# Kernel tuning notes

Measured on AMD Instinct MI355X. Metric: run time of the kernel, lower is better.

Reference implementation:

```python
import jax, jax.numpy as jnp
import numpy as np

DIM = 1024
HEADS = 16
HD = DIM // HEADS  # 64
EPS = 1.1920928955078125e-07  # torch.finfo(float32).eps, RMSNorm default


def setup_inputs() -> dict:
    key = jax.random.key(0)
    ks = jax.random.split(key, 8)
    s = 0.02
    return {
        "x": jax.random.normal(ks[0], (2, 2048, DIM), jnp.float32),
        "pe": jax.random.normal(ks[1], (1, 1, 2048, HD // 2, 2, 2), jnp.float32),
        "qkv_w": jax.random.normal(ks[2], (3 * DIM, DIM), jnp.float32) * s,
        "qkv_b": jax.random.normal(ks[3], (3 * DIM,), jnp.float32) * s,
        "q_norm_w": jnp.ones((HD,), jnp.float32),
        "k_norm_w": jnp.ones((HD,), jnp.float32),
        "proj_w": jax.random.normal(ks[4], (DIM, DIM), jnp.float32) * s,
        "proj_b": jax.random.normal(ks[5], (DIM,), jnp.float32) * s,
    }


def _rms_norm(t, w):
    var = jnp.mean(jnp.square(t), axis=-1, keepdims=True)
    return t * jax.lax.rsqrt(var + EPS) * w


def _apply_rope(t, pe):
    # t: [B,H,L,D]; pe: [1,1,L,D/2,2,2]
    B, H, L, D = t.shape
    tp = t.reshape(B, H, L, D // 2, 1, 2)
    out = pe[..., 0] * tp[..., 0] + pe[..., 1] * tp[..., 1]  # [B,H,L,D/2,2]
    return out.reshape(B, H, L, D)


def reference(x, pe, qkv_w, qkv_b, q_norm_w, k_norm_w, proj_w, proj_b):
    B, L, _ = x.shape
    qkv = x @ qkv_w.T + qkv_b  # [B,L,3*DIM]
    qkv = qkv.reshape(B, L, 3, HEADS, HD).transpose(2, 0, 3, 1, 4)  # [3,B,H,L,D]
    q, k, v = qkv[0], qkv[1], qkv[2]
    q = _rms_norm(q, q_norm_w)
    k = _rms_norm(k, k_norm_w)
    q = _apply_rope(q, pe)
    k = _apply_rope(k, pe)
    scale = 1.0 / np.sqrt(HD).astype(np.float32)
    scores = jnp.einsum("bhqd,bhkd->bhqk", q, k) * scale  # [B,H,L,L]
    attn = jax.nn.softmax(scores, axis=-1)
    o = jnp.einsum("bhqk,bhkd->bhqd", attn, v)  # [B,H,L,D]
    o = o.transpose(0, 2, 1, 3).reshape(B, L, DIM)  # B L (H D)
    return o @ proj_w.T + proj_b
```

## Files before the change

### kernel.cpp

```cpp
#include <hip/hip_runtime.h>
#include <hip/hip_bf16.h>

#define DIM   1024
#define HEADS 16
#define HD    64
#define BB    2
#define LL    2048
#define MTOT  (BB*LL)
#define EPSV  1.1920928955078125e-07f

typedef __attribute__((ext_vector_type(8))) short bf16x8;
typedef __attribute__((ext_vector_type(4))) float f32x4;
typedef unsigned short ushort_t;

__device__ __forceinline__ float bf2f(ushort_t u) {
    unsigned int x = ((unsigned int)u) << 16;
    return __builtin_bit_cast(float, x);
}
__device__ __forceinline__ ushort_t f2bf(float f) {
    unsigned int x = __builtin_bit_cast(unsigned int, f);
    unsigned int r = (x + 0x7FFFu + ((x >> 16) & 1u)) >> 16;
    return (ushort_t)r;
}

__global__ __launch_bounds__(256) void f32_to_bf16_k(const float* __restrict__ in,
                                                     ushort_t* __restrict__ out, int n) {
    int i = (blockIdx.x * 256 + threadIdx.x) * 4;
    if (i < n) {
        float4 v = *(const float4*)(in + i);
        ushort4 o;
        o.x = f2bf(v.x); o.y = f2bf(v.y); o.z = f2bf(v.z); o.w = f2bf(v.w);
        *(ushort4*)(out + i) = o;
    }
}

__global__ __launch_bounds__(512, 2) void gemm256(const ushort_t* __restrict__ A,
                                                  const ushort_t* __restrict__ Bt,
                                                  const float* __restrict__ bias,
                                                  ushort_t* __restrict__ C,
                                                  int M, int N, int K) {
    __shared__ __attribute__((aligned(16))) ushort_t Asm[2][256 * 64];
    __shared__ __attribute__((aligned(16))) ushort_t Bsm[2][256 * 64];
    const int tid = threadIdx.x;
    const int lane = tid & 63, wid = tid >> 6;
    const int wm = wid >> 1, wn = wid & 1;
    const int r = lane & 15, g = lane >> 4;

    const int mtiles = M >> 8;
    const int cpx = gridDim.x >> 3;
    const int bid = blockIdx.x;
    const int swz = (bid & 7) * cpx + (bid >> 3);
    const int mt = swz % mtiles, nt = swz / mtiles;
    const int m0 = mt * 256, n0 = nt * 256;

    int srow[2], sgx[2];
#pragma unroll
    for (int q = 0; q < 2; ++q) {
        int c = q * 512 + tid;
        srow[q] = c >> 3;
        sgx[q] = ((c & 7) ^ (srow[q] & 7)) * 8;
    }
    const ushort_t* pa[2][2];
    const ushort_t* pb[2][2];
#pragma unroll
    for (int q = 0; q < 2; ++q)
#pragma unroll
        for (int h = 0; h < 2; ++h) {
            pa[q][h] = A + (size_t)(m0 + h * 128 + srow[q]) * K + sgx[q];
            pb[q][h] = Bt + (size_t)(n0 + h * 128 + srow[q]) * K + sgx[q];
        }

    f32x4 acc[4][8] = {};

    auto stage = [&](int kt, int slot) {
        const int kc = kt * 64;
#pragma unroll
        for (int h = 0; h < 2; ++h)
#pragma unroll
            for (int q = 0; q < 2; ++q) {
                __builtin_amdgcn_global_load_lds(
                    (const __attribute__((address_space(1))) void*)(pa[q][h] + kc),
                    (__attribute__((address_space(3))) void*)(&Asm[slot][0] + h * 8192 + (q * 512 + wid * 64) * 8),
                    16, 0, 0);
                __builtin_amdgcn_global_load_lds(
                    (const __attribute__((address_space(1))) void*)(pb[q][h] + kc),
                    (__attribute__((address_space(3))) void*)(&Bsm[slot][0] + h * 8192 + (q * 512 + wid * 64) * 8),
                    16, 0, 0);
            }
    };

    stage(0, 0);
    asm volatile("s_waitcnt vmcnt(0)" ::: "memory");
    __builtin_amdgcn_s_barrier();
    asm volatile("" ::: "memory");

    const int nkt = K >> 6;
    for (int kt = 0; kt < nkt; ++kt) {
        const int slot = kt & 1;
        if (kt + 1 < nkt) stage(kt + 1, slot ^ 1);
        const ushort_t* As = &Asm[slot][0];
        const ushort_t* Bs = &Bsm[slot][0];
#pragma unroll
        for (int ks = 0; ks < 2; ++ks) {
            bf16x8 af[4], bf[8];
#pragma unroll
            for (int mi = 0; mi < 4; ++mi) {
                int row = wm * 64 + mi * 16 + r;
                af[mi] = *(const bf16x8*)(As + row * 64 + (((ks * 4 + g) * 8) ^ ((row & 7) * 8)));
            }
#pragma unroll
            for (int ni = 0; ni < 8; ++ni) {
                int row = wn * 128 + ni * 16 + r;
                bf[ni] = *(const bf16x8*)(Bs + row * 64 + (((ks * 4 + g) * 8) ^ ((row & 7) * 8)));
            }
            __builtin_amdgcn_s_setprio(1);
#pragma unroll
            for (int mi = 0; mi < 4; ++mi)
#pragma unroll
                for (int ni = 0; ni < 8; ++ni)
                    acc[mi][ni] = __builtin_amdgcn_mfma_f32_16x16x32_bf16(af[mi], bf[ni], acc[mi][ni], 0, 0, 0);
            __builtin_amdgcn_s_setprio(0);
        }
        asm volatile("s_waitcnt vmcnt(0)" ::: "memory");
        __builtin_amdgcn_s_barrier();
        asm volatile("" ::: "memory");
    }

#pragma unroll
    for (int ni = 0; ni < 8; ++ni) {
        int col = n0 + wn * 128 + ni * 16 + r;
        float bv = bias[col];
#pragma unroll
        for (int mi = 0; mi < 4; ++mi)
#pragma unroll
            for (int reg = 0; reg < 4; ++reg) {
                int row = m0 + wm * 64 + mi * 16 + g * 4 + reg;
                C[(size_t)row * N + col] = f2bf(acc[mi][ni][reg] + bv);
            }
    }
}

template <int OUT_BF16>
__global__ __launch_bounds__(256) void gemm_bt(const ushort_t* __restrict__ A,
                                               const ushort_t* __restrict__ Bt,
                                               const float* __restrict__ bias,
                                               void* __restrict__ Cout,
                                               int M, int N, int K) {
    __shared__ __attribute__((aligned(16))) ushort_t Asm[128 * 32];
    __shared__ __attribute__((aligned(16))) ushort_t Bsm[128 * 32];
    int tid = threadIdx.x;
    int lane = tid & 63, wid = tid >> 6;
    int wm = wid >> 1, wn = wid & 1;
    int r = lane & 15, g = lane >> 4;
    int m0 = blockIdx.y * 128, n0 = blockIdx.x * 128;

    f32x4 acc[4][4] = {};

    int niter = K >> 5;
    for (int kk = 0; kk < niter; ++kk) {
        int k0 = kk << 5;
        __syncthreads();
#pragma unroll
        for (int p = 0; p < 2; ++p) {
            int off = (p * 256 + tid) * 8;
            int row = off >> 5, col = off & 31;
            int ldsoff = (p * 256 + wid * 64) * 8;
            __builtin_amdgcn_global_load_lds(
                (const __attribute__((address_space(1))) void*)(A + (size_t)(m0 + row) * K + k0 + col),
                (__attribute__((address_space(3))) void*)(Asm + ldsoff), 16, 0, 0);
            __builtin_amdgcn_global_load_lds(
                (const __attribute__((address_space(1))) void*)(Bt + (size_t)(n0 + row) * K + k0 + col),
                (__attribute__((address_space(3))) void*)(Bsm + ldsoff), 16, 0, 0);
        }
        __syncthreads();
        bf16x8 af[4], bfr[4];
#pragma unroll
        for (int mi = 0; mi < 4; mi++)
            af[mi] = *(const bf16x8*)(Asm + (wm * 64 + mi * 16 + r) * 32 + g * 8);
#pragma unroll
        for (int ni = 0; ni < 4; ni++)
            bfr[ni] = *(const bf16x8*)(Bsm + (wn * 64 + ni * 16 + r) * 32 + g * 8);
#pragma unroll
        for (int mi = 0; mi < 4; mi++)
#pragma unroll
            for (int ni = 0; ni < 4; ni++)
                acc[mi][ni] = __builtin_amdgcn_mfma_f32_16x16x32_bf16(af[mi], bfr[ni], acc[mi][ni], 0, 0, 0);
    }
#pragma unroll
    for (int mi = 0; mi < 4; mi++)
#pragma unroll
        for (int ni = 0; ni < 4; ni++) {
            int col = n0 + wn * 64 + ni * 16 + r;
            float bv = bias[col];
#pragma unroll
            for (int reg = 0; reg < 4; reg++) {
                int row = m0 + wm * 64 + mi * 16 + g * 4 + reg;
                float v = acc[mi][ni][reg] + bv;
                if (OUT_BF16)
                    ((ushort_t*)Cout)[(size_t)row * N + col] = f2bf(v);
                else
                    ((float*)Cout)[(size_t)row * N + col] = v;
            }
        }
}

__global__ __launch_bounds__(256) void norm_rope_k(const ushort_t* __restrict__ qkv,
                                                   const float* __restrict__ pe,
                                                   const float* __restrict__ qnw,
                                                   const float* __restrict__ knw,
                                                   ushort_t* __restrict__ qh,
                                                   ushort_t* __restrict__ kh,
                                                   ushort_t* __restrict__ vT) {
    __shared__ ushort_t T[64][68];
    const int tid = threadIdx.x;
    const int lane = tid & 63, w = tid >> 6;
    const int rg = lane >> 4;
    const int d4 = (lane & 15) * 4;
    const int l0 = blockIdx.x * 64;
    const int t  = blockIdx.y;
    const int bh = blockIdx.z;
    const int b = bh >> 4, h = bh & 15;

    if (t == 2) {
#pragma unroll
        for (int i = 0; i < 4; ++i) {
            int ll = w * 16 + rg + 4 * i;
            int m = b * 2048 + l0 + ll;
            ushort4 v = *(const ushort4*)(qkv + (size_t)m * 3072 + 2048 + h * 64 + d4);
            *(ushort4*)(&T[ll][d4]) = v;
        }
        __syncthreads();
        const int d = tid >> 2, lq = (tid & 3) * 16;
        ushort_t* dst = vT + ((size_t)(bh * 64 + d)) * 2048 + l0 + lq;
#pragma unroll
        for (int c = 0; c < 4; ++c) {
            ushort4 o;
            o.x = T[lq + c * 4 + 0][d];
            o.y = T[lq + c * 4 + 1][d];
            o.z = T[lq + c * 4 + 2][d];
            o.w = T[lq + c * 4 + 3][d];
            *(ushort4*)(dst + c * 4) = o;
        }
        return;
    }

    const float* nwp = (t == 0) ? qnw : knw;
    const float4 nwv = *(const float4*)(nwp + d4);
    ushort_t* dst = (t == 0) ? qh : kh;
    const float qscale = (t == 0) ? 0.125f : 1.0f;
#pragma unroll
    for (int i = 0; i < 4; ++i) {
        int ll = w * 16 + rg + 4 * i;
        int l = l0 + ll;
        int m = b * 2048 + l;
        ushort4 vv = *(const ushort4*)(qkv + (size_t)m * 3072 + t * 1024 + h * 64 + d4);
        float v0 = bf2f(vv.x), v1 = bf2f(vv.y), v2 = bf2f(vv.z), v3 = bf2f(vv.w);
        float ss = v0 * v0 + v1 * v1 + v2 * v2 + v3 * v3;
        ss += __shfl_xor(ss, 1, 64);
        ss += __shfl_xor(ss, 2, 64);
        ss += __shfl_xor(ss, 4, 64);
        ss += __shfl_xor(ss, 8, 64);
        float rms = rsqrtf(ss * (1.0f / 64.0f) + EPSV);
        v0 *= rms * nwv.x; v1 *= rms * nwv.y; v2 *= rms * nwv.z; v3 *= rms * nwv.w;
        float4 p0 = *(const float4*)(pe + (size_t)l * 128 + 2 * d4);
        float4 p1 = *(const float4*)(pe + (size_t)l * 128 + 2 * d4 + 4);
        float o0 = (p0.x * v0 + p0.y * v1) * qscale;
        float o1 = (p0.z * v0 + p0.w * v1) * qscale;
        float o2 = (p1.x * v2 + p1.y * v3) * qscale;
        float o3 = (p1.z * v2 + p1.w * v3) * qscale;
        ushort4 o;
        o.x = f2bf(o0); o.y = f2bf(o1); o.z = f2bf(o2); o.w = f2bf(o3);
        *(ushort4*)(dst + ((size_t)bh * 2048 + l) * 64 + d4) = o;
    }
}

__global__ __launch_bounds__(256, 2) void attn_k(const ushort_t* __restrict__ qh,
                                                 const ushort_t* __restrict__ kh,
                                                 const ushort_t* __restrict__ vT,
                                                 ushort_t* __restrict__ ob) {
    __shared__ __attribute__((aligned(16))) ushort_t Ksm[2][64 * 64];
    __shared__ __attribute__((aligned(16))) ushort_t Vsm[2][64 * 64];
    __shared__ __attribute__((aligned(16))) ushort_t Plds[4][2][16 * 64];

    const int tid = threadIdx.x;
    const int lane = tid & 63, wid = tid >> 6;
    const int r = lane & 15, g = lane >> 4;
    const int qt = blockIdx.x, bh = blockIdx.y;
    const int q0 = qt * 128 + wid * 32;
    const ushort_t* Q  = qh + (size_t)bh * LL * 64;
    const ushort_t* Kb = kh + (size_t)bh * LL * 64;
    const ushort_t* Vt = vT + (size_t)bh * 64 * LL;

    int row_[2], ccx_[2];
#pragma unroll
    for (int q = 0; q < 2; ++q) {
        int c = q * 256 + tid;
        row_[q] = c >> 3;
        ccx_[q] = (c & 7) ^ (row_[q] & 7);
    }
    const int swz = (r & 7) * 8;

    bf16x8 qf[2][2];
#pragma unroll
    for (int mf = 0; mf < 2; ++mf)
#pragma unroll
        for (int hf = 0; hf < 2; ++hf)
            qf[mf][hf] = *(const bf16x8*)(Q + (size_t)(q0 + mf * 16 + r) * 64 + hf * 32 + g * 8);

    f32x4 acc[2][4] = {};
    float mrow[2] = {-1e30f, -1e30f};
    float srow[2] = {0.f, 0.f};
    const f32x4 zero = {};

#pragma unroll
    for (int q = 0; q < 2; ++q) {
        __builtin_amdgcn_global_load_lds(
            (const __attribute__((address_space(1))) void*)(Kb + (size_t)row_[q] * 64 + ccx_[q] * 8),
            (__attribute__((address_space(3))) void*)(&Ksm[0][0] + (q * 256 + wid * 64) * 8), 16, 0, 0);
        __builtin_amdgcn_global_load_lds(
            (const __attribute__((address_space(1))) void*)(Vt + (size_t)row_[q] * 2048 + ccx_[q] * 8),
            (__attribute__((address_space(3))) void*)(&Vsm[0][0] + (q * 256 + wid * 64) * 8), 16, 0, 0);
    }
    __syncthreads();

    int buf = 0;
    for (int it = 0; it < 32; ++it) {
        if (it < 31) {
            int kvn = (it + 1) * 64;
#pragma unroll
            for (int q = 0; q < 2; ++q) {
                __builtin_amdgcn_global_load_lds(
                    (const __attribute__((address_space(1))) void*)(Kb + (size_t)(kvn + row_[q]) * 64 + ccx_[q] * 8),
                    (__attribute__((address_space(3))) void*)(&Ksm[buf ^ 1][0] + (q * 256 + wid * 64) * 8), 16, 0, 0);
                __builtin_amdgcn_global_load_lds(
                    (const __attribute__((address_space(1))) void*)(Vt + (size_t)row_[q] * 2048 + kvn + ccx_[q] * 8),
                    (__attribute__((address_space(3))) void*)(&Vsm[buf ^ 1][0] + (q * 256 + wid * 64) * 8), 16, 0, 0);
            }
        }
        const ushort_t* Kl = &Ksm[buf][0];
        const ushort_t* Vl = &Vsm[buf][0];

        bf16x8 kf[4][2];
#pragma unroll
        for (int kt = 0; kt < 4; ++kt)
#pragma unroll
            for (int hf = 0; hf < 2; ++hf)
                kf[kt][hf] = *(const bf16x8*)(Kl + (kt * 16 + r) * 64 + (((hf * 4 + g) * 8) ^ swz));

        f32x4 s[2][4];
        __builtin_amdgcn_s_setprio(1);
#pragma unroll
        for (int mf = 0; mf < 2; ++mf)
#pragma unroll
            for (int kt = 0; kt < 4; ++kt) {
                f32x4 t0 = __builtin_amdgcn_mfma_f32_16x16x32_bf16(kf[kt][0], qf[mf][0], zero, 0, 0, 0);
                s[mf][kt] = __builtin_amdgcn_mfma_f32_16x16x32_bf16(kf[kt][1], qf[mf][1], t0, 0, 0, 0);
            }
        __builtin_amdgcn_s_setprio(0);

#pragma unroll
        for (int mf = 0; mf < 2; ++mf) {
            float pm = -1e30f;
#pragma unroll
            for (int kt = 0; kt < 4; ++kt)
#pragma unroll
                for (int reg = 0; reg < 4; ++reg) pm = fmaxf(pm, s[mf][kt][reg]);
            pm = fmaxf(pm, __shfl_xor(pm, 16, 64));
            pm = fmaxf(pm, __shfl_xor(pm, 32, 64));
            bool skip = (__all(pm <= mrow[mf] + 8.0f) != 0);
            float mn, al;
            if (skip) {
                mn = mrow[mf];
            } else {
                mn = fmaxf(mrow[mf], pm);
                al = __expf(mrow[mf] - mn);
                mrow[mf] = mn;
            }
            float rs = 0.f;
#pragma unroll
            for (int kt = 0; kt < 4; ++kt)
#pragma unroll
                for (int reg = 0; reg < 4; ++reg) {
                    float p = __expf(s[mf][kt][reg] - mn);
                    s[mf][kt][reg] = p;
                    rs += p;
                }
            rs += __shfl_xor(rs, 16, 64);
            rs += __shfl_xor(rs, 32, 64);
            if (skip) {
                srow[mf] += rs;
            } else {
                srow[mf] = srow[mf] * al + rs;
                float ab[4];
#pragma unroll
                for (int reg = 0; reg < 4; ++reg) ab[reg] = __shfl(al, g * 4 + reg, 16);
#pragma unroll
                for (int dt = 0; dt < 4; ++dt)
#pragma unroll
                    for (int reg = 0; reg < 4; ++reg) acc[mf][dt][reg] *= ab[reg];
            }
#pragma unroll
            for (int kt = 0; kt < 4; ++kt) {
                ushort4 pw;
                pw.x = f2bf(s[mf][kt][0]); pw.y = f2bf(s[mf][kt][1]);
                pw.z = f2bf(s[mf][kt][2]); pw.w = f2bf(s[mf][kt][3]);
                *(ushort4*)(&Plds[wid][mf][0] + r * 64 + (((2 * kt + (g >> 1)) * 8) ^ swz) + (g & 1) * 4) = pw;
            }
        }
        asm volatile("s_waitcnt lgkmcnt(0)" ::: "memory");
        __builtin_amdgcn_sched_barrier(0);

        bf16x8 pa[2][2];
#pragma unroll
        for (int mf = 0; mf < 2; ++mf)
#pragma unroll
            for (int hf = 0; hf < 2; ++hf)
                pa[mf][hf] = *(const bf16x8*)(&Plds[wid][mf][0] + r * 64 + (((hf * 4 + g) * 8) ^ swz));

        __builtin_amdgcn_s_setprio(1);
#pragma unroll
        for (int dt = 0; dt < 4; ++dt)
#pragma unroll
            for (int hv = 0; hv < 2; ++hv) {
                bf16x8 vf = *(const bf16x8*)(Vl + (dt * 16 + r) * 64 + (((hv * 4 + g) * 8) ^ swz));
#pragma unroll
                for (int mf = 0; mf < 2; ++mf)
                    acc[mf][dt] = __builtin_amdgcn_mfma_f32_16x16x32_bf16(pa[mf][hv], vf, acc[mf][dt], 0, 0, 0);
            }
        __builtin_amdgcn_s_setprio(0);

        __syncthreads();
        buf ^= 1;
    }

    int b = bh >> 4, h = bh & 15;
#pragma unroll
    for (int mf = 0; mf < 2; ++mf) {
        float sinv = 1.0f / srow[mf];
        float sb[4];
#pragma unroll
        for (int reg = 0; reg < 4; ++reg) sb[reg] = __shfl(sinv, g * 4 + reg, 16);
#pragma unroll
        for (int dt = 0; dt < 4; ++dt)
#pragma unroll
            for (int reg = 0; reg < 4; ++reg) {
                int l = q0 + mf * 16 + g * 4 + reg;
                ob[((size_t)(b * 2048 + l)) * 1024 + h * 64 + dt * 16 + r] =
                    f2bf(acc[mf][dt][reg] * sb[reg]);
            }
    }
}

extern "C" void kernel_launch(void* const* d_in, const int* in_sizes, int n_in,
                              void* d_out, int out_size, void* d_ws, size_t ws_size,
                              hipStream_t stream) {
    const float* x      = (const float*)d_in[0];
    const float* pe     = (const float*)d_in[1];
    const float* qkv_w  = (const float*)d_in[2];
    const float* qkv_b  = (const float*)d_in[3];
    const float* qnw    = (const float*)d_in[4];
    const float* knw    = (const float*)d_in[5];
    const float* proj_w = (const float*)d_in[6];
    const float* proj_b = (const float*)d_in[7];
    float* out = (float*)d_out;

    char* ws = (char*)d_ws;
    ushort_t* xb    = (ushort_t*)(ws);
    ushort_t* wqkv  = (ushort_t*)(ws + 8388608);
    ushort_t* wproj = (ushort_t*)(ws + 8388608 + 6291456);
    ushort_t* qkvb  = (ushort_t*)(ws + 16777216);
    ushort_t* qhp   = (ushort_t*)(ws + 16777216 + 25165824);
    ushort_t* khp   = (ushort_t*)(ws + 16777216 + 25165824 + 8388608);
    ushort_t* vtp   = (ushort_t*)(ws + 16777216 + 25165824 + 2 * 8388608);
    ushort_t* obp   = qkvb;

    f32_to_bf16_k<<<MTOT * DIM / 1024, 256, 0, stream>>>(x, xb, MTOT * DIM);
    f32_to_bf16_k<<<3 * DIM * DIM / 1024, 256, 0, stream>>>(qkv_w, wqkv, 3 * DIM * DIM);
    f32_to_bf16_k<<<DIM * DIM / 1024, 256, 0, stream>>>(proj_w, wproj, DIM * DIM);

    gemm256<<<(MTOT / 256) * (3 * DIM / 256), 512, 0, stream>>>(xb, wqkv, qkv_b, qkvb,
                                                                MTOT, 3 * DIM, DIM);
    norm_rope_k<<<dim3(32, 3, 32), 256, 0, stream>>>(qkvb, pe, qnw, knw, qhp, khp, vtp);
    attn_k<<<dim3(16, 32), 256, 0, stream>>>(qhp, khp, vtp, obp);
    gemm_bt<0><<<dim3(DIM / 128, MTOT / 128), 256, 0, stream>>>(obp, wproj, proj_b, out,
                                                                MTOT, DIM, DIM);
}
```

Measured before the change: 234.6 us.

## Retile QKV and projection GEMMs, merge conversions, pack bf16 converts in attention

The three fp32-to-bf16 conversion launches become one kernel. The 256x256 QKV GEMM is replaced by a 128x128 double-buffered tile kernel, giving 768 blocks instead of 192 for better CU coverage. The projection GEMM gains a 128x64 tile with a 64-wide K step, swizzled LDS and double buffering, producing 512 blocks. The attention kernel now packs P to bf16 with v_cvt_pk_bf16_f32. In exchange, smaller tiles lower per-block arithmetic intensity and raise global/LDS traffic per FLOP.

Result: faster. 217.6 us (-7.2%).

```diff
diff --git a/kernel.cpp b/kernel.cpp
--- a/kernel.cpp
+++ b/kernel.cpp
@@ -22,71 +22,71 @@
     unsigned int r = (x + 0x7FFFu + ((x >> 16) & 1u)) >> 16;
     return (ushort_t)r;
 }
-
-__global__ __launch_bounds__(256) void f32_to_bf16_k(const float* __restrict__ in,
-                                                     ushort_t* __restrict__ out, int n) {
+__device__ __forceinline__ unsigned int cvt_pk_bf16(float lo, float hi) {
+    unsigned int r;
+    asm("v_cvt_pk_bf16_f32 %0, %1, %2" : "=v"(r) : "v"(lo), "v"(hi));
+    return r;
+}
+
+__global__ __launch_bounds__(256) void cvt_all_k(const float* __restrict__ a, int na,
+                                                 const float* __restrict__ b, int nb,
+                                                 const float* __restrict__ c,
+                                                 ushort_t* __restrict__ oa,
+                                                 ushort_t* __restrict__ ob,
+                                                 ushort_t* __restrict__ oc) {
     int i = (blockIdx.x * 256 + threadIdx.x) * 4;
-    if (i < n) {
-        float4 v = *(const float4*)(in + i);
-        ushort4 o;
-        o.x = f2bf(v.x); o.y = f2bf(v.y); o.z = f2bf(v.z); o.w = f2bf(v.w);
-        *(ushort4*)(out + i) = o;
-    }
-}
-
-__global__ __launch_bounds__(512, 2) void gemm256(const ushort_t* __restrict__ A,
+    const float* src;
+    ushort_t* dst;
+    int off;
+    if (i < na)            { src = a; dst = oa; off = i; }
+    else if (i < na + nb)  { src = b; dst = ob; off = i - na; }
+    else                   { src = c; dst = oc; off = i - na - nb; }
+    float4 v = *(const float4*)(src + off);
+    ushort4 o;
+    o.x = f2bf(v.x); o.y = f2bf(v.y); o.z = f2bf(v.z); o.w = f2bf(v.w);
+    *(ushort4*)(dst + off) = o;
+}
+
+__global__ __launch_bounds__(256, 2) void gemm128(const ushort_t* __restrict__ A,
                                                   const ushort_t* __restrict__ Bt,
                                                   const float* __restrict__ bias,
                                                   ushort_t* __restrict__ C,
                                                   int M, int N, int K) {
-    __shared__ __attribute__((aligned(16))) ushort_t Asm[2][256 * 64];
-    __shared__ __attribute__((aligned(16))) ushort_t Bsm[2][256 * 64];
+    __shared__ __attribute__((aligned(16))) ushort_t Asm[2][128 * 64];
+    __shared__ __attribute__((aligned(16))) ushort_t Bsm[2][128 * 64];
     const int tid = threadIdx.x;
     const int lane = tid & 63, wid = tid >> 6;
     const int wm = wid >> 1, wn = wid & 1;
     const int r = lane & 15, g = lane >> 4;
-
-    const int mtiles = M >> 8;
-    const int cpx = gridDim.x >> 3;
-    const int bid = blockIdx.x;
-    const int swz = (bid & 7) * cpx + (bid >> 3);
-    const int mt = swz % mtiles, nt = swz / mtiles;
-    const int m0 = mt * 256, n0 = nt * 256;
-
-    int srow[2], sgx[2];
-#pragma unroll
-    for (int q = 0; q < 2; ++q) {
-        int c = q * 512 + tid;
-        srow[q] = c >> 3;
-        sgx[q] = ((c & 7) ^ (srow[q] & 7)) * 8;
-    }
-    const ushort_t* pa[2][2];
-    const ushort_t* pb[2][2];
-#pragma unroll
-    for (int q = 0; q < 2; ++q)
-#pragma unroll
-        for (int h = 0; h < 2; ++h) {
-            pa[q][h] = A + (size_t)(m0 + h * 128 + srow[q]) * K + sgx[q];
-            pb[q][h] = Bt + (size_t)(n0 + h * 128 + srow[q]) * K + sgx[q];
-        }
-
-    f32x4 acc[4][8] = {};
+    const int m0 = blockIdx.y * 128, n0 = blockIdx.x * 128;
+
+    int srow[4], sgx[4];
+#pragma unroll
+    for (int p = 0; p < 4; ++p) {
+        int c = p * 256 + tid;
+        srow[p] = c >> 3;
+        sgx[p] = ((c & 7) ^ (srow[p] & 7)) * 8;
+    }
+    const ushort_t *pa[4], *pb[4];
+#pragma unroll
+    for (int p = 0; p < 4; ++p) {
+        pa[p] = A + (size_t)(m0 + srow[p]) * K + sgx[p];
+        pb[p] = Bt + (size_t)(n0 + srow[p]) * K + sgx[p];
+    }
+
+    f32x4 acc[4][4] = {};
 
     auto stage = [&](int kt, int slot) {
         const int kc = kt * 64;
 #pragma unroll
-        for (int h = 0; h < 2; ++h)
-#pragma unroll
-            for (int q = 0; q < 2; ++q) {
-                __builtin_amdgcn_global_load_lds(
-                    (const __attribute__((address_space(1))) void*)(pa[q][h] + kc),
-                    (__attribute__((address_space(3))) void*)(&Asm[slot][0] + h * 8192 + (q * 512 + wid * 64) * 8),
-                    16, 0, 0);
-                __builtin_amdgcn_global_load_lds(
-                    (const __attribute__((address_space(1))) void*)(pb[q][h] + kc),
-                    (__attribute__((address_space(3))) void*)(&Bsm[slot][0] + h * 8192 + (q * 512 + wid * 64) * 8),
-                    16, 0, 0);
-            }
+        for (int p = 0; p < 4; ++p) {
+            __builtin_amdgcn_global_load_lds(
+                (const __attribute__((address_space(1))) void*)(pa[p] + kc),
+                (__attribute__((address_space(3))) void*)(&Asm[slot][0] + (p * 256 + wid * 64) * 8), 16, 0, 0);
+            __builtin_amdgcn_global_load_lds(
+                (const __attribute__((address_space(1))) void*)(pb[p] + kc),
+                (__attribute__((address_space(3))) void*)(&Bsm[slot][0] + (p * 256 + wid * 64) * 8), 16, 0, 0);
+        }
     };
 
     stage(0, 0);
@@ -102,22 +102,22 @@
         const ushort_t* Bs = &Bsm[slot][0];
 #pragma unroll
         for (int ks = 0; ks < 2; ++ks) {
-            bf16x8 af[4], bf[8];
+            bf16x8 af[4], bf[4];
 #pragma unroll
             for (int mi = 0; mi < 4; ++mi) {
                 int row = wm * 64 + mi * 16 + r;
-                af[mi] = *(const bf16x8*)(As + row * 64 + (((ks * 4 + g) * 8) ^ ((row & 7) * 8)));
-            }
-#pragma unroll
-            for (int ni = 0; ni < 8; ++ni) {
-                int row = wn * 128 + ni * 16 + r;
-                bf[ni] = *(const bf16x8*)(Bs + row * 64 + (((ks * 4 + g) * 8) ^ ((row & 7) * 8)));
+                af[mi] = *(const bf16x8*)(As + row * 64 + (((ks * 4 + g) ^ (row & 7)) * 8));
+            }
+#pragma unroll
+            for (int ni = 0; ni < 4; ++ni) {
+                int row = wn * 64 + ni * 16 + r;
+                bf[ni] = *(const bf16x8*)(Bs + row * 64 + (((ks * 4 + g) ^ (row & 7)) * 8));
             }
             __builtin_amdgcn_s_setprio(1);
 #pragma unroll
             for (int mi = 0; mi < 4; ++mi)
 #pragma unroll
-                for (int ni = 0; ni < 8; ++ni)
+                for (int ni = 0; ni < 4; ++ni)
                     acc[mi][ni] = __builtin_amdgcn_mfma_f32_16x16x32_bf16(af[mi], bf[ni], acc[mi][ni], 0, 0, 0);
             __builtin_amdgcn_s_setprio(0);
         }
@@ -127,66 +127,6 @@
     }
 
 #pragma unroll
-    for (int ni = 0; ni < 8; ++ni) {
-        int col = n0 + wn * 128 + ni * 16 + r;
-        float bv = bias[col];
-#pragma unroll
-        for (int mi = 0; mi < 4; ++mi)
-#pragma unroll
-            for (int reg = 0; reg < 4; ++reg) {
-                int row = m0 + wm * 64 + mi * 16 + g * 4 + reg;
-                C[(size_t)row * N + col] = f2bf(acc[mi][ni][reg] + bv);
-            }
-    }
-}
-
-template <int OUT_BF16>
-__global__ __launch_bounds__(256) void gemm_bt(const ushort_t* __restrict__ A,
-                                               const ushort_t* __restrict__ Bt,
-                                               const float* __restrict__ bias,
-                                               void* __restrict__ Cout,
-                                               int M, int N, int K) {
-    __shared__ __attribute__((aligned(16))) ushort_t Asm[128 * 32];
-    __shared__ __attribute__((aligned(16))) ushort_t Bsm[128 * 32];
-    int tid = threadIdx.x;
-    int lane = tid & 63, wid = tid >> 6;
-    int wm = wid >> 1, wn = wid & 1;
-    int r = lane & 15, g = lane >> 4;
-    int m0 = blockIdx.y * 128, n0 = blockIdx.x * 128;
-
-    f32x4 acc[4][4] = {};
-
-    int niter = K >> 5;
-    for (int kk = 0; kk < niter; ++kk) {
-        int k0 = kk << 5;
-        __syncthreads();
-#pragma unroll
-        for (int p = 0; p < 2; ++p) {
-            int off = (p * 256 + tid) * 8;
-            int row = off >> 5, col = off & 31;
-            int ldsoff = (p * 256 + wid * 64) * 8;
-            __builtin_amdgcn_global_load_lds(
-                (const __attribute__((address_space(1))) void*)(A + (size_t)(m0 + row) * K + k0 + col),
-                (__attribute__((address_space(3))) void*)(Asm + ldsoff), 16, 0, 0);
-            __builtin_amdgcn_global_load_lds(
-                (const __attribute__((address_space(1))) void*)(Bt + (size_t)(n0 + row) * K + k0 + col),
-                (__attribute__((address_space(3))) void*)(Bsm + ldsoff), 16, 0, 0);
-        }
-        __syncthreads();
-        bf16x8 af[4], bfr[4];
-#pragma unroll
-        for (int mi = 0; mi < 4; mi++)
-            af[mi] = *(const bf16x8*)(Asm + (wm * 64 + mi * 16 + r) * 32 + g * 8);
-#pragma unroll
-        for (int ni = 0; ni < 4; ni++)
-            bfr[ni] = *(const bf16x8*)(Bsm + (wn * 64 + ni * 16 + r) * 32 + g * 8);
-#pragma unroll
-        for (int mi = 0; mi < 4; mi++)
-#pragma unroll
-            for (int ni = 0; ni < 4; ni++)
-                acc[mi][ni] = __builtin_amdgcn_mfma_f32_16x16x32_bf16(af[mi], bfr[ni], acc[mi][ni], 0, 0, 0);
-    }
-#pragma unroll
     for (int mi = 0; mi < 4; mi++)
 #pragma unroll
         for (int ni = 0; ni < 4; ni++) {
@@ -195,11 +135,100 @@
 #pragma unroll
             for (int reg = 0; reg < 4; reg++) {
                 int row = m0 + wm * 64 + mi * 16 + g * 4 + reg;
-                float v = acc[mi][ni][reg] + bv;
-                if (OUT_BF16)
-                    ((ushort_t*)Cout)[(size_t)row * N + col] = f2bf(v);
-                else
-                    ((float*)Cout)[(size_t)row * N + col] = v;
+                C[(size_t)row * N + col] = f2bf(acc[mi][ni][reg] + bv);
+            }
+        }
+}
+
+__global__ __launch_bounds__(256, 2) void gemm_pj(const ushort_t* __restrict__ A,
+                                                  const ushort_t* __restrict__ Bt,
+                                                  const float* __restrict__ bias,
+                                                  float* __restrict__ C,
+                                                  int M, int N, int K) {
+    __shared__ __attribute__((aligned(16))) ushort_t Asm[2][128 * 64];
+    __shared__ __attribute__((aligned(16))) ushort_t Bsm[2][64 * 64];
+    const int tid = threadIdx.x;
+    const int lane = tid & 63, wid = tid >> 6;
+    const int wm = wid >> 1, wn = wid & 1;
+    const int r = lane & 15, g = lane >> 4;
+    const int m0 = blockIdx.y * 128, n0 = blockIdx.x * 64;
+
+    int srow[4], sgx[4];
+#pragma unroll
+    for (int p = 0; p < 4; ++p) {
+        int c = p * 256 + tid;
+        srow[p] = c >> 3;
+        sgx[p] = ((c & 7) ^ (srow[p] & 7)) * 8;
+    }
+    const ushort_t *pa[4], *pb[2];
+#pragma unroll
+    for (int p = 0; p < 4; ++p) pa[p] = A + (size_t)(m0 + srow[p]) * K + sgx[p];
+#pragma unroll
+    for (int p = 0; p < 2; ++p) pb[p] = Bt + (size_t)(n0 + srow[p]) * K + sgx[p];
+
+    f32x4 acc[4][2] = {};
+
+    auto stage = [&](int kt, int slot) {
+        const int kc = kt * 64;
+#pragma unroll
+        for (int p = 0; p < 4; ++p)
+            __builtin_amdgcn_global_load_lds(
+                (const __attribute__((address_space(1))) void*)(pa[p] + kc),
+                (__attribute__((address_space(3))) void*)(&Asm[slot][0] + (p * 256 + wid * 64) * 8), 16, 0, 0);
+#pragma unroll
+        for (int p = 0; p < 2; ++p)
+            __builtin_amdgcn_global_load_lds(
+                (const __attribute__((address_space(1))) void*)(pb[p] + kc),
+                (__attribute__((address_space(3))) void*)(&Bsm[slot][0] + (p * 256 + wid * 64) * 8), 16, 0, 0);
+    };
+
+    stage(0, 0);
+    asm volatile("s_waitcnt vmcnt(0)" ::: "memory");
+    __builtin_amdgcn_s_barrier();
+    asm volatile("" ::: "memory");
+
+    const int nkt = K >> 6;
+    for (int kt = 0; kt < nkt; ++kt) {
+        const int slot = kt & 1;
+        if (kt + 1 < nkt) stage(kt + 1, slot ^ 1);
+        const ushort_t* As = &Asm[slot][0];
+        const ushort_t* Bs = &Bsm[slot][0];
+#pragma unroll
+        for (int ks = 0; ks < 2; ++ks) {
+            bf16x8 af[4], bf[2];
+#pragma unroll
+            for (int mi = 0; mi < 4; ++mi) {
+                int row = wm * 64 + mi * 16 + r;
+                af[mi] = *(const bf16x8*)(As + row * 64 + (((ks * 4 + g) ^ (row & 7)) * 8));
+            }
+#pragma unroll
+            for (int ni = 0; ni < 2; ++ni) {
+                int row = wn * 32 + ni * 16 + r;
+                bf[ni] = *(const bf16x8*)(Bs + row * 64 + (((ks * 4 + g) ^ (row & 7)) * 8));
+            }
+            __builtin_amdgcn_s_setprio(1);
+#pragma unroll
+            for (int mi = 0; mi < 4; ++mi)
+#pragma unroll
+                for (int ni = 0; ni < 2; ++ni)
+                    acc[mi][ni] = __builtin_amdgcn_mfma_f32_16x16x32_bf16(af[mi], bf[ni], acc[mi][ni], 0, 0, 0);
+            __builtin_amdgcn_s_setprio(0);
+        }
+        asm volatile("s_waitcnt vmcnt(0)" ::: "memory");
+        __builtin_amdgcn_s_barrier();
+        asm volatile("" ::: "memory");
+    }
+
+#pragma unroll
+    for (int mi = 0; mi < 4; mi++)
+#pragma unroll
+        for (int ni = 0; ni < 2; ni++) {
+            int col = n0 + wn * 32 + ni * 16 + r;
+            float bv = bias[col];
+#pragma unroll
+            for (int reg = 0; reg < 4; reg++) {
+                int row = m0 + wm * 64 + mi * 16 + g * 4 + reg;
+                C[(size_t)row * N + col] = acc[mi][ni][reg] + bv;
             }
         }
 }
@@ -401,10 +430,10 @@
             }
 #pragma unroll
             for (int kt = 0; kt < 4; ++kt) {
-                ushort4 pw;
-                pw.x = f2bf(s[mf][kt][0]); pw.y = f2bf(s[mf][kt][1]);
-                pw.z = f2bf(s[mf][kt][2]); pw.w = f2bf(s[mf][kt][3]);
-                *(ushort4*)(&Plds[wid][mf][0] + r * 64 + (((2 * kt + (g >> 1)) * 8) ^ swz) + (g & 1) * 4) = pw;
+                uint2 pw;
+                pw.x = cvt_pk_bf16(s[mf][kt][0], s[mf][kt][1]);
+                pw.y = cvt_pk_bf16(s[mf][kt][2], s[mf][kt][3]);
+                *(uint2*)((ushort_t*)&Plds[wid][mf][0] + r * 64 + (((2 * kt + (g >> 1)) * 8) ^ swz) + (g & 1) * 4) = pw;
             }
         }
         asm volatile("s_waitcnt lgkmcnt(0)" ::: "memory");
@@ -474,14 +503,14 @@
     ushort_t* vtp   = (ushort_t*)(ws + 16777216 + 25165824 + 2 * 8388608);
     ushort_t* obp   = qkvb;
 
-    f32_to_bf16_k<<<MTOT * DIM / 1024, 256, 0, stream>>>(x, xb, MTOT * DIM);
-    f32_to_bf16_k<<<3 * DIM * DIM / 1024, 256, 0, stream>>>(qkv_w, wqkv, 3 * DIM * DIM);
-    f32_to_bf16_k<<<DIM * DIM / 1024, 256, 0, stream>>>(proj_w, wproj, DIM * DIM);
-
-    gemm256<<<(MTOT / 256) * (3 * DIM / 256), 512, 0, stream>>>(xb, wqkv, qkv_b, qkvb,
-                                                                MTOT, 3 * DIM, DIM);
+    const int na = MTOT * DIM, nb = 3 * DIM * DIM, nc = DIM * DIM;
+    cvt_all_k<<<(na + nb + nc) / 1024, 256, 0, stream>>>(x, na, qkv_w, nb, proj_w,
+                                                         xb, wqkv, wproj);
+
+    gemm128<<<dim3(3 * DIM / 128, MTOT / 128), 256, 0, stream>>>(xb, wqkv, qkv_b, qkvb,
+                                                                 MTOT, 3 * DIM, DIM);
     norm_rope_k<<<dim3(32, 3, 32), 256, 0, stream>>>(qkvb, pe, qnw, knw, qhp, khp, vtp);
     attn_k<<<dim3(16, 32), 256, 0, stream>>>(qhp, khp, vtp, obp);
-    gemm_bt<0><<<dim3(DIM / 128, MTOT / 128), 256, 0, stream>>>(obp, wproj, proj_b, out,
-                                                                MTOT, DIM, DIM);
-}
+    gemm_pj<<<dim3(DIM / 64, MTOT / 128), 256, 0, stream>>>(obp, wproj, proj_b, out,
+                                                            MTOT, DIM, DIM);
+}
```
